# Performance work log

Hardware: AMD Instinct MI355X
Metric: run time of the kernel (lower is better)

Reference implementation:

```python
import jax, jax.numpy as jnp
import numpy as np

NUM_HOSTS = 13


def gcn_conv_max(x, src, dst, n, W, b):
    """PyG GCNConv with aggr='max': x@W, gcn_norm (self-loops + sym norm), max-scatter, +bias.
    src/dst already include self-loop edges."""
    xw = x @ W  # [N, out]
    deg = jnp.zeros((n,), xw.dtype).at[dst].add(1.0)
    dinv = jax.lax.rsqrt(deg)  # deg >= 1 thanks to self-loops
    norm = dinv[src] * dinv[dst]  # [E+N]
    msg = norm[:, None] * xw[src]  # [E+N, out] -- the big gather
    agg = jax.ops.segment_max(msg, dst, num_segments=n)
    return agg + b


def self_attn(v, g, aW, ab, fW, fb, gW, gb):
    """SimpleSelfAttention: softmax over feature dim, weighted-sum over nodes, residual global update."""
    att = jax.nn.softmax(v @ aW + ab, axis=-1)  # [B, Nh, h]
    feat = v @ fW + fb                            # [B, Nh, h]
    out = jnp.sum(att * feat, axis=1)             # [B, h]
    g_ = jnp.concatenate([out, g], axis=-1) @ gW + gb
    return g + g_


def setup_inputs() -> dict:
    key = jax.random.key(0)
    ks = jax.random.split(key, 24)
    IN, H1, H2 = 64, 256, 64
    B, NPG = 256, 200
    N = B * NPG
    E = 409600

    x = jax.random.normal(ks[0], (N, IN), jnp.float32)
    host_idx = (jnp.arange(B)[:, None] * NPG + jnp.arange(NUM_HOSTS)[None, :]).reshape(-1).astype(jnp.int32)
    x = x.at[host_idx, 0].set(1.0)  # hosts = x[:,0]==1
    ei = jax.random.randint(ks[1], (2, E), 0, N, dtype=jnp.int64)

    def lin(k, i, o):
        k1, k2 = jax.random.split(k)
        s = 1.0 / np.sqrt(i)
        return (jax.random.uniform(k1, (i, o), jnp.float32, -s, s),
                jax.random.uniform(k2, (o,), jnp.float32, -s, s))

    W1, b1 = lin(ks[2], IN, H1)
    W2, b2 = lin(ks[3], H1, H2)
    # g0: in=IN, h=H1, g=H1 ; g1: in=H1, h=H1 ; g2: in=H2, h=H2
    a0W, a0b = lin(ks[4], IN, H1); f0W, f0b = lin(ks[5], IN, H1); g0W, g0b = lin(ks[6], H1 + H1, H1)
    a1W, a1b = lin(ks[7], H1, H1); f1W, f1b = lin(ks[8], H1, H1); g1W, g1b = lin(ks[9], H1 + H1, H1)
    a2W, a2b = lin(ks[10], H2, H2); f2W, f2b = lin(ks[11], H2, H2); g2W, g2b = lin(ks[12], H2 + H1, H1)
    o1W, o1b = lin(ks[13], H1, H2)
    o2W, o2b = lin(ks[14], H2, 1)

    return dict(x=x, ei=ei, host_idx=host_idx,
                W1=W1, b1=b1, W2=W2, b2=b2,
                a0W=a0W, a0b=a0b, f0W=f0W, f0b=f0b, g0W=g0W, g0b=g0b,
                a1W=a1W, a1b=a1b, f1W=f1W, f1b=f1b, g1W=g1W, g1b=g1b,
                a2W=a2W, a2b=a2b, f2W=f2W, f2b=f2b, g2W=g2W, g2b=g2b,
                o1W=o1W, o1b=o1b, o2W=o2W, o2b=o2b)


def reference(x, ei, host_idx,
              W1, b1, W2, b2,
              a0W, a0b, f0W, f0b, g0W, g0b,
              a1W, a1b, f1W, f1b, g1W, g1b,
              a2W, a2b, f2W, f2b, g2W, g2b,
              o1W, o1b, o2W, o2b):
    n = x.shape[0]
    B = host_idx.shape[0] // NUM_HOSTS
    loops = jnp.arange(n, dtype=ei.dtype)
    src = jnp.concatenate([ei[0], loops])
    dst = jnp.concatenate([ei[1], loops])

    hx = x[host_idx].reshape(B, NUM_HOSTS, -1)
    g = self_attn(hx, jnp.zeros((B, g0b.shape[0]), x.dtype), a0W, a0b, f0W, f0b, g0W, g0b)

    x1 = jax.nn.relu(gcn_conv_max(x, src, dst, n, W1, b1))
    g = self_attn(x1[host_idx].reshape(B, NUM_HOSTS, -1), g, a1W, a1b, f1W, f1b, g1W, g1b)

    x2 = jax.nn.relu(gcn_conv_max(x1, src, dst, n, W2, b2))
    g = self_attn(x2[host_idx].reshape(B, NUM_HOSTS, -1), g, a2W, a2b, f2W, f2b, g2W, g2b)

    return jax.nn.relu(g @ o1W + o1b) @ o2W + o2b  # [B, 1]
```

## Files before the change

### kernel.cpp

```cpp
#include <hip/hip_runtime.h>
#include <math.h>
#include <stdio.h>

#define N_NODES 51200
#define N_EDGES 409600
#define B_GRAPH 256
#define NH 13

typedef float v4f __attribute__((ext_vector_type(4)));
typedef unsigned v2u __attribute__((ext_vector_type(2)));
__device__ __forceinline__ void nt_store_u2(uint2* p, uint2 v) {
    v2u w; w.x = v.x; w.y = v.y;
    __builtin_nontemporal_store(w, (v2u*)p);
}

__device__ __forceinline__ unsigned pack_bf2(float a, float b) {
    unsigned ua = __float_as_uint(a);
    ua = (ua + 0x7fffu + ((ua >> 16) & 1u)) >> 16;
    unsigned ub = __float_as_uint(b);
    ub = (ub + 0x7fffu + ((ub >> 16) & 1u)) & 0xffff0000u;
    return ua | ub;
}
__device__ __forceinline__ float bf_lo(unsigned u) { return __uint_as_float(u << 16); }
__device__ __forceinline__ float bf_hi(unsigned u) { return __uint_as_float(u & 0xffff0000u); }

__device__ __forceinline__ bool ei_is_64(const int* __restrict__ ei32) {
    int z = 1;
    #pragma unroll
    for (int k = 1; k < 16; k += 2) z &= (ei32[k] == 0);
    return z != 0;
}

__global__ void count_deg(const int* __restrict__ ei32, const long long* __restrict__ ei64,
                          int* __restrict__ degc) {
    int e = blockIdx.x * 256 + threadIdx.x;
    if (e >= N_EDGES) return;
    int v = ei_is_64(ei32) ? (int)ei64[N_EDGES + e] : ei32[N_EDGES + e];
    atomicAdd(&degc[v], 1);
}

__global__ void scan_block_sums(const int* __restrict__ degc, int* __restrict__ bsums) {
    __shared__ int sdata[256];
    int i = blockIdx.x * 256 + threadIdx.x;
    sdata[threadIdx.x] = degc[i];
    __syncthreads();
    for (int s = 128; s > 0; s >>= 1) {
        if (threadIdx.x < s) sdata[threadIdx.x] += sdata[threadIdx.x + s];
        __syncthreads();
    }
    if (threadIdx.x == 0) bsums[blockIdx.x] = sdata[0];
}

__global__ void scan_finalize(int* __restrict__ degc, int* __restrict__ offs,
                              float* __restrict__ dinv, const int* __restrict__ bsums) {
    __shared__ int bs[256];
    __shared__ int s[256];
    const int t = threadIdx.x;
    bs[t] = (t < 200) ? bsums[t] : 0;
    __syncthreads();
    for (int off = 1; off < 256; off <<= 1) {
        int u = (t >= off) ? bs[t - off] : 0;
        __syncthreads();
        bs[t] += u;
        __syncthreads();
    }
    int i = blockIdx.x * 256 + t;
    int cnt = degc[i];
    s[t] = cnt;
    __syncthreads();
    for (int off = 1; off < 256; off <<= 1) {
        int u = (t >= off) ? s[t - off] : 0;
        __syncthreads();
        s[t] += u;
        __syncthreads();
    }
    int base = (blockIdx.x == 0) ? 0 : bs[blockIdx.x - 1];
    int excl = base + s[t] - cnt;
    offs[i] = excl;
    dinv[i] = rsqrtf((float)(cnt + 1));
    degc[i] = excl;
    if (i == N_NODES - 1) offs[N_NODES] = N_EDGES;
}

template <int K, int WS, bool BF16IN>
__device__ __forceinline__ void gemm_body64(const float* __restrict__ X,
        const float* __restrict__ W, const float* __restrict__ bias,
        float* __restrict__ Y, int row0, const int* __restrict__ rows,
        float* __restrict__ xs, float* __restrict__ ws) {
    constexpr int BK = 32;
    constexpr int XS = BK + 4;
    const int t = threadIdx.x;
    const int ct = t & 15;
    const int rt = t >> 4;
    float acc[4][4] = {{0.f}};
    for (int kc = 0; kc < K; kc += BK) {
        __syncthreads();
        #pragma unroll
        for (int i = 0; i < 2; ++i) {
            int idx = t + i * 256;
            int q = idx & 7, r = idx >> 3;
            int xr = rows[r];
            float4 v;
            if (BF16IN) {
                uint2 pv = ((const uint2*)X)[(size_t)xr * (K / 4) + kc / 4 + q];
                v = make_float4(bf_lo(pv.x), bf_hi(pv.x), bf_lo(pv.y), bf_hi(pv.y));
            } else {
                v = *(const float4*)(X + (size_t)xr * K + kc + q * 4);
            }
            *(float4*)&xs[r * XS + q * 4] = v;
        }
        #pragma unroll
        for (int i = 0; i < 2; ++i) {
            int idx = t + i * 256;
            int q = idx & 15, k = idx >> 4;
            float4 v = *(const float4*)(W + (size_t)(kc + k) * WS + q * 4);
            *(float4*)&ws[k * 64 + q * 4] = v;
        }
        __syncthreads();
        #pragma unroll
        for (int kb = 0; kb < BK; kb += 4) {
            float4 wv[4];
            #pragma unroll
            for (int kk = 0; kk < 4; ++kk)
                wv[kk] = *(const float4*)&ws[(kb + kk) * 64 + ct * 4];
            #pragma unroll
            for (int r = 0; r < 4; ++r) {
                float4 xv = *(const float4*)&xs[(rt * 4 + r) * XS + kb];
                float xk[4] = {xv.x, xv.y, xv.z, xv.w};
                #pragma unroll
                for (int kk = 0; kk < 4; ++kk) {
                    acc[r][0] = fmaf(xk[kk], wv[kk].x, acc[r][0]);
                    acc[r][1] = fmaf(xk[kk], wv[kk].y, acc[r][1]);
                    acc[r][2] = fmaf(xk[kk], wv[kk].z, acc[r][2]);
                    acc[r][3] = fmaf(xk[kk], wv[kk].w, acc[r][3]);
                }
            }
        }
    }
    #pragma unroll
    for (int r = 0; r < 4; ++r) {
        int row = row0 + rt * 4 + r;
        float4 o = make_float4(acc[r][0] + bias[ct * 4 + 0],
                               acc[r][1] + bias[ct * 4 + 1],
                               acc[r][2] + bias[ct * 4 + 2],
                               acc[r][3] + bias[ct * 4 + 3]);
        *(float4*)&Y[(size_t)row * 512 + ct * 4] = o;
    }
}

template <int K, int WS, int YS, bool BF16OUT>
__device__ __forceinline__ void gemm_main64(const float* __restrict__ X,
        const float* __restrict__ W, const float* __restrict__ dinv,
        float* __restrict__ Y, int row0,
        float* __restrict__ xs, float* __restrict__ ws) {
    constexpr int BK = 32;
    constexpr int XS = BK + 4;
    const int t = threadIdx.x;
    const int ct = t & 15;
    const int rt = t >> 4;
    float acc[4][4] = {{0.f}};
    for (int kc = 0; kc < K; kc += BK) {
        __syncthreads();
        #pragma unroll
        for (int i = 0; i < 2; ++i) {
            int idx = t + i * 256;
            int q = idx & 7, r = idx >> 3;
            float4 v = *(const float4*)(X + (size_t)(row0 + r) * K + kc + q * 4);
            *(float4*)&xs[r * XS + q * 4] = v;
        }
        #pragma unroll
        for (int i = 0; i < 2; ++i) {
            int idx = t + i * 256;
            int q = idx & 15, k = idx >> 4;
            float4 v = *(const float4*)(W + (size_t)(kc + k) * WS + q * 4);
            *(float4*)&ws[k * 64 + q * 4] = v;
        }
        __syncthreads();
        #pragma unroll
        for (int kb = 0; kb < BK; kb += 4) {
            float4 wv[4];
            #pragma unroll
            for (int kk = 0; kk < 4; ++kk)
                wv[kk] = *(const float4*)&ws[(kb + kk) * 64 + ct * 4];
            #pragma unroll
            for (int r = 0; r < 4; ++r) {
                float4 xv = *(const float4*)&xs[(rt * 4 + r) * XS + kb];
                float xk[4] = {xv.x, xv.y, xv.z, xv.w};
                #pragma unroll
                for (int kk = 0; kk < 4; ++kk) {
                    acc[r][0] = fmaf(xk[kk], wv[kk].x, acc[r][0]);
                    acc[r][1] = fmaf(xk[kk], wv[kk].y, acc[r][1]);
                    acc[r][2] = fmaf(xk[kk], wv[kk].z, acc[r][2]);
                    acc[r][3] = fmaf(xk[kk], wv[kk].w, acc[r][3]);
                }
            }
        }
    }
    #pragma unroll
    for (int r = 0; r < 4; ++r) {
        int row = row0 + rt * 4 + r;
        float sc = dinv[row];
        float4 o = make_float4(acc[r][0] * sc, acc[r][1] * sc,
                               acc[r][2] * sc, acc[r][3] * sc);
        if (BF16OUT) {
            unsigned short* yb = (unsigned short*)Y + (size_t)row * YS;
            uint2 pk;
            pk.x = pack_bf2(o.x, o.y);
            pk.y = pack_bf2(o.z, o.w);
            ((uint2*)yb)[ct] = pk;
        } else {
            *(float4*)&Y[(size_t)row * YS + ct * 4] = o;
        }
    }
}

template <int K, int WS, int YS, int NCOLB, int CPT, bool BF16IN, bool BF16OUT>
__device__ __forceinline__ void gemm_main(const float* __restrict__ X,
        const float* __restrict__ W, const float* __restrict__ dinv,
        float* __restrict__ Y, int row0,
        float* __restrict__ xs, float* __restrict__ ws) {
    constexpr int BK = 32;
    constexpr int XS = BK + 4;
    constexpr int CQ = CPT / 4;
    const int t = threadIdx.x;
    const int ct = t & 15;
    const int rt = t >> 4;
    float acc[8][CPT];
    #pragma unroll
    for (int r = 0; r < 8; ++r)
        #pragma unroll
        for (int c = 0; c < CPT; ++c) acc[r][c] = 0.f;
    for (int kc = 0; kc < K; kc += BK) {
        __syncthreads();
        #pragma unroll
        for (int i = 0; i < 4; ++i) {
            int idx = t + i * 256;
            int q = idx & 7, r = idx >> 3;
            float4 v;
            if (BF16IN) {
                uint2 pv = ((const uint2*)X)[(size_t)(row0 + r) * (K / 4) + kc / 4 + q];
                v = make_float4(bf_lo(pv.x), bf_hi(pv.x), bf_lo(pv.y), bf_hi(pv.y));
            } else {
                v = *(const float4*)(X + (size_t)(row0 + r) * K + kc + q * 4);
            }
            *(float4*)&xs[r * XS + q * 4] = v;
        }
        #pragma unroll
        for (int i = 0; i < NCOLB / 32; ++i) {
            int idx = t + i * 256;
            int q = idx & (NCOLB / 4 - 1), k = idx / (NCOLB / 4);
            float4 v = *(const float4*)(W + (size_t)(kc + k) * WS + q * 4);
            *(float4*)&ws[k * NCOLB + q * 4] = v;
        }
        __syncthreads();
        #pragma unroll
        for (int kb = 0; kb < BK; kb += 4) {
            float4 wv[4][CQ];
            #pragma unroll
            for (int kk = 0; kk < 4; ++kk)
                #pragma unroll
                for (int cq = 0; cq < CQ; ++cq)
                    wv[kk][cq] = *(const float4*)&ws[(kb + kk) * NCOLB + cq * 64 + ct * 4];
            #pragma unroll
            for (int r = 0; r < 8; ++r) {
                float4 xv = *(const float4*)&xs[(rt + 16 * r) * XS + kb];
                float xk[4] = {xv.x, xv.y, xv.z, xv.w};
                #pragma unroll
                for (int kk = 0; kk < 4; ++kk)
                    #pragma unroll
                    for (int cq = 0; cq < CQ; ++cq) {
                        acc[r][cq * 4 + 0] = fmaf(xk[kk], wv[kk][cq].x, acc[r][cq * 4 + 0]);
                        acc[r][cq * 4 + 1] = fmaf(xk[kk], wv[kk][cq].y, acc[r][cq * 4 + 1]);
                        acc[r][cq * 4 + 2] = fmaf(xk[kk], wv[kk][cq].z, acc[r][cq * 4 + 2]);
                        acc[r][cq * 4 + 3] = fmaf(xk[kk], wv[kk][cq].w, acc[r][cq * 4 + 3]);
                    }
            }
        }
    }
    #pragma unroll
    for (int r = 0; r < 8; ++r) {
        int row = row0 + rt + 16 * r;
        float sc = dinv[row];
        #pragma unroll
        for (int cq = 0; cq < CQ; ++cq) {
            float4 o = make_float4(acc[r][cq * 4 + 0] * sc, acc[r][cq * 4 + 1] * sc,
                                   acc[r][cq * 4 + 2] * sc, acc[r][cq * 4 + 3] * sc);
            if (BF16OUT) {
                unsigned short* yb = (unsigned short*)Y + (size_t)row * YS;
                uint2 pk;
                pk.x = pack_bf2(o.x, o.y);
                pk.y = pack_bf2(o.z, o.w);
                ((uint2*)yb)[cq * 16 + ct] = pk;
            } else {
                *(float4*)&Y[(size_t)row * YS + cq * 64 + ct * 4] = o;
            }
        }
    }
}

__global__ __launch_bounds__(256) void fused_gemm1(const float* __restrict__ x,
        const float* __restrict__ W1, float* __restrict__ xw1b,
        const float* __restrict__ dinv,
        const int* __restrict__ ei32, const long long* __restrict__ ei64,
        int* __restrict__ cursor, int* __restrict__ csr,
        const int* __restrict__ host_idx,
        const float* __restrict__ a0W, const float* __restrict__ a0b,
        const float* __restrict__ f0W, const float* __restrict__ f0b,
        float* __restrict__ AF) {
    __shared__ float xs[64 * 36];
    __shared__ float ws[32 * 64];
    __shared__ int rows[64];
    const int bid = blockIdx.x;
    const int t = threadIdx.x;
    if (bid < 3200) {
        const int rb = bid >> 2;
        const int cb = bid & 3;
        gemm_main64<64, 256, 256, true>(
            x, W1 + cb * 64, dinv, xw1b + cb * 32, rb * 64, xs, ws);
    } else if (bid < 3616) {
        const int abid = bid - 3200;
        const int rb = abid >> 3;
        const int cb = abid & 7;
        const int c0 = cb * 64;
        const float* Wp = (c0 < 256) ? (a0W + c0) : (f0W + (c0 - 256));
        const float* bp = (c0 < 256) ? (a0b + c0) : (f0b + (c0 - 256));
        if (t < 64) rows[t] = host_idx[rb * 64 + t];
        __syncthreads();
        gemm_body64<64, 256, false>(x, Wp, bp, AF + c0, rb * 64, rows, xs, ws);
    } else {
        int e = (bid - 3616) * 256 + t;
        if (e < N_EDGES) {
            int u, v;
            if (ei_is_64(ei32)) { u = (int)ei64[e]; v = (int)ei64[N_EDGES + e]; }
            else                { u = ei32[e];      v = ei32[N_EDGES + e]; }
            int pos = atomicAdd(&cursor[v], 1);
            csr[pos] = u;
        }
    }
}

__global__ __launch_bounds__(256) void fused_gemm2(const float* __restrict__ x1b,
        const float* __restrict__ W2, float* __restrict__ xw2,
        const float* __restrict__ dinv,
        const int* __restrict__ host_idx,
        const float* __restrict__ a1W, const float* __restrict__ a1b,
        const float* __restrict__ f1W, const float* __restrict__ f1b,
        float* __restrict__ AF) {
    __shared__ float xs[128 * 36];
    __shared__ float ws[32 * 64];
    __shared__ int rows[64];
    const int bid = blockIdx.x;
    const int t = threadIdx.x;
    if (bid < 400) {
        gemm_main<256, 64, 64, 64, 4, true, false>(
            x1b, W2, dinv, xw2, bid * 128, xs, ws);
    } else {
        const int abid = bid - 400;
        const int rb = abid >> 3;
        const int cb = abid & 7;
        const int c0 = cb * 64;
        const float* Wp = (c0 < 256) ? (a1W + c0) : (f1W + (c0 - 256));
        const float* bp = (c0 < 256) ? (a1b + c0) : (f1b + (c0 - 256));
        if (t < 64) rows[t] = host_idx[rb * 64 + t];
        __syncthreads();
        gemm_body64<256, 256, true>(x1b, Wp, bp, AF + c0, rb * 64, rows, xs, ws);
    }
}

__device__ __forceinline__ void attn_red256(const float* __restrict__ AF,
        const float* __restrict__ gW, const float* __restrict__ gb,
        const float* __restrict__ g_in, float* __restrict__ g_out, int b,
        float (*At)[256], float* red_m, float* red_s, float* cat) {
    const int t = threadIdx.x;
    const int wave = t >> 6, lane = t & 63;
    float accA[NH], accF[NH];
    #pragma unroll
    for (int j = 0; j < NH; ++j) {
        const float* r = AF + (size_t)(b * NH + j) * 512;
        accA[j] = r[t];
        accF[j] = r[256 + t];
        At[j][t] = accA[j];
    }
    __syncthreads();
    for (int j = wave; j < NH; j += 4) {
        float m = -3.402823466e38f;
        #pragma unroll
        for (int q = 0; q < 4; ++q) m = fmaxf(m, At[j][q * 64 + lane]);
        #pragma unroll
        for (int off = 32; off; off >>= 1) m = fmaxf(m, __shfl_xor(m, off));
        if (lane == 0) red_m[j] = m;
    }
    __syncthreads();
    #pragma unroll
    for (int j = 0; j < NH; ++j) At[j][t] = expf(accA[j] - red_m[j]);
    __syncthreads();
    for (int j = wave; j < NH; j += 4) {
        float s = 0.f;
        #pragma unroll
        for (int q = 0; q < 4; ++q) s += At[j][q * 64 + lane];
        #pragma unroll
        for (int off = 32; off; off >>= 1) s += __shfl_xor(s, off);
        if (lane == 0) red_s[j] = s;
    }
    __syncthreads();
    float outc = 0.f;
    #pragma unroll
    for (int j = 0; j < NH; ++j) outc += At[j][t] / red_s[j] * accF[j];
    cat[t] = outc;
    float gv = g_in ? g_in[b * 256 + t] : 0.f;
    cat[256 + t] = gv;
    __syncthreads();
    float acc = gb[t];
    const float* gwp = gW + t;
    #pragma unroll 4
    for (int i4 = 0; i4 < 128; ++i4) {
        float4 cq = ((const float4*)cat)[i4];
        const float* gw4 = gwp + (size_t)i4 * 4 * 256;
        acc = fmaf(cq.x, gw4[0], acc);
        acc = fmaf(cq.y, gw4[256], acc);
        acc = fmaf(cq.z, gw4[512], acc);
        acc = fmaf(cq.w, gw4[768], acc);
    }
    g_out[b * 256 + t] = gv + acc;
}

__global__ __launch_bounds__(256) void fused_agg256(const uint2* __restrict__ xwb,
        const float* __restrict__ dinv, const int* __restrict__ offs,
        const int* __restrict__ csr, const float* __restrict__ bias,
        uint2* __restrict__ outb,
        const float* __restrict__ AF, const float* __restrict__ gW,
        const float* __restrict__ gb, const float* __restrict__ g_in,
        float* __restrict__ g_out) {
    __shared__ float At[NH][256];
    __shared__ float red_m[NH];
    __shared__ float red_s[NH];
    __shared__ float cat[512];
    const int bid = blockIdx.x;
    if (bid < 256) {
        attn_red256(AF, gW, gb, g_in, g_out, bid, At, red_m, red_s, cat);
        return;
    }
    int gid = (bid - 256) * 256 + threadIdx.x;
    int v = gid >> 6;
    int lane = gid & 63;
    uint2 sw = xwb[(size_t)v * 64 + lane];
    float4 acc = make_float4(bf_lo(sw.x), bf_hi(sw.x), bf_lo(sw.y), bf_hi(sw.y));
    int e0 = offs[v];
    int e1 = offs[v + 1];
    int em = e0 + ((e1 - e0) & ~7);
    for (int e = e0; e < em; e += 8) {
        int u[8];
        #pragma unroll
        for (int i = 0; i < 8; ++i) u[i] = csr[e + i];
        uint2 m[8];
        #pragma unroll
        for (int i = 0; i < 8; ++i) m[i] = xwb[(size_t)u[i] * 64 + lane];
        #pragma unroll
        for (int i = 0; i < 8; ++i) {
            acc.x = fmaxf(acc.x, bf_lo(m[i].x));
            acc.y = fmaxf(acc.y, bf_hi(m[i].x));
            acc.z = fmaxf(acc.z, bf_lo(m[i].y));
            acc.w = fmaxf(acc.w, bf_hi(m[i].y));
        }
    }
    if (em < e1) {
        int u[8];
        #pragma unroll
        for (int i = 0; i < 8; ++i) u[i] = csr[(em + i < e1) ? (em + i) : (e1 - 1)];
        uint2 m[8];
        #pragma unroll
        for (int i = 0; i < 8; ++i) m[i] = xwb[(size_t)u[i] * 64 + lane];
        #pragma unroll
        for (int i = 0; i < 8; ++i) {
            if (em + i < e1) {
                acc.x = fmaxf(acc.x, bf_lo(m[i].x));
                acc.y = fmaxf(acc.y, bf_hi(m[i].x));
                acc.z = fmaxf(acc.z, bf_lo(m[i].y));
                acc.w = fmaxf(acc.w, bf_hi(m[i].y));
            }
        }
    }
    float dv = dinv[v];
    float4 b4 = ((const float4*)bias)[lane];
    float4 o;
    o.x = fmaxf(fmaf(acc.x, dv, b4.x), 0.f);
    o.y = fmaxf(fmaf(acc.y, dv, b4.y), 0.f);
    o.z = fmaxf(fmaf(acc.z, dv, b4.z), 0.f);
    o.w = fmaxf(fmaf(acc.w, dv, b4.w), 0.f);
    uint2 pk;
    pk.x = pack_bf2(o.x, o.y);
    pk.y = pack_bf2(o.z, o.w);
    nt_store_u2(outb + (size_t)v * 64 + lane, pk);
}

__global__ __launch_bounds__(1024) void attn_graph_head(
        const float* __restrict__ AF,
        const float* __restrict__ g1W, const float* __restrict__ g1b,
        const float* __restrict__ g_in,
        const float* __restrict__ xw2,
        const float* __restrict__ dinv, const int* __restrict__ offs,
        const int* __restrict__ csr, const float* __restrict__ b2,
        const int* __restrict__ host_idx,
        const float* __restrict__ a2W, const float* __restrict__ a2b,
        const float* __restrict__ f2W, const float* __restrict__ f2b,
        const float* __restrict__ g2W, const float* __restrict__ g2b,
        const float* __restrict__ o1W, const float* __restrict__ o1b,
        const float* __restrict__ o2W, const float* __restrict__ o2b,
        float* __restrict__ out) {
    __shared__ float At[NH][256];
    __shared__ float Ft[NH][256];
    __shared__ float red_m[NH];
    __shared__ float red_s[NH];
    __shared__ float cat[512];
    __shared__ float catB[320];
    __shared__ float g1s[256];
    __shared__ float x2l[NH][64];
    __shared__ float part4[4][256];
    __shared__ float part16[16][64];
    __shared__ float grow[256];
    const int b = blockIdx.x;
    const int t = threadIdx.x;
    const int wave = t >> 6;
    const int lane = t & 63;
    const int c = t & 255;
    const int quad = t >> 8;

    if (wave < NH) {
        int hv = host_idx[b * NH + wave];
        float acc = xw2[(size_t)hv * 64 + lane];
        int e0 = offs[hv], e1 = offs[hv + 1];
        for (int e = e0; e < e1; e += 8) {
            int u[8];
            #pragma unroll
            for (int i = 0; i < 8; ++i) u[i] = csr[(e + i < e1) ? (e + i) : (e1 - 1)];
            float m[8];
            #pragma unroll
            for (int i = 0; i < 8; ++i) m[i] = xw2[(size_t)u[i] * 64 + lane];
            #pragma unroll
            for (int i = 0; i < 8; ++i)
                if (e + i < e1) acc = fmaxf(acc, m[i]);
        }
        x2l[wave][lane] = fmaxf(fmaf(acc, dinv[hv], b2[lane]), 0.f);
    }
    for (int idx = t; idx < NH * 128; idx += 1024) {
        int j = idx >> 7, q = idx & 127;
        float4 v = ((const float4*)(AF + (size_t)(b * NH + j) * 512))[q];
        if (q < 64) *(float4*)&At[j][q * 4] = v;
        else        *(float4*)&Ft[j][(q - 64) * 4] = v;
    }
    __syncthreads();
    if (wave < NH) {
        float m = -3.402823466e38f;
        #pragma unroll
        for (int q = 0; q < 4; ++q) m = fmaxf(m, At[wave][q * 64 + lane]);
        #pragma unroll
        for (int off = 32; off; off >>= 1) m = fmaxf(m, __shfl_xor(m, off));
        if (lane == 0) red_m[wave] = m;
    }
    __syncthreads();
    for (int idx = t; idx < NH * 256; idx += 1024) {
        int j = idx >> 8, cc = idx & 255;
        At[j][cc] = expf(At[j][cc] - red_m[j]);
    }
    __syncthreads();
    if (wave < NH) {
        float s = 0.f;
        #pragma unroll
        for (int q = 0; q < 4; ++q) s += At[wave][q * 64 + lane];
        #pragma unroll
        for (int off = 32; off; off >>= 1) s += __shfl_xor(s, off);
        if (lane == 0) red_s[wave] = s;
    }
    __syncthreads();
    if (quad == 0) {
        float outc = 0.f;
        #pragma unroll
        for (int j = 0; j < NH; ++j) outc += At[j][c] / red_s[j] * Ft[j][c];
        cat[c] = outc;
        cat[256 + c] = g_in[b * 256 + c];
    }
    __syncthreads();
    {
        float acc = 0.f;
        const float* gwp = g1W + c;
        #pragma unroll 4
        for (int i4 = quad * 32; i4 < quad * 32 + 32; ++i4) {
            float4 cq = ((const float4*)cat)[i4];
            const float* gw4 = gwp + (size_t)i4 * 1024;
            acc = fmaf(cq.x, gw4[0], acc);
            acc = fmaf(cq.y, gw4[256], acc);
            acc = fmaf(cq.z, gw4[512], acc);
            acc = fmaf(cq.w, gw4[768], acc);
        }
        part4[quad][c] = acc;
    }
    __syncthreads();
    if (quad == 0)
        g1s[c] = cat[256 + c] + g1b[c] +
                 part4[0][c] + part4[1][c] + part4[2][c] + part4[3][c];
    __syncthreads();
    if (wave < NH) {
        float aA = a2b[lane], aF = f2b[lane];
        #pragma unroll 8
        for (int k = 0; k < 64; ++k) {
            float xv = x2l[wave][k];
            aA = fmaf(xv, a2W[k * 64 + lane], aA);
            aF = fmaf(xv, f2W[k * 64 + lane], aF);
        }
        float m = aA;
        #pragma unroll
        for (int off = 32; off; off >>= 1) m = fmaxf(m, __shfl_xor(m, off));
        float pexp = expf(aA - m);
        float s = pexp;
        #pragma unroll
        for (int off = 32; off; off >>= 1) s += __shfl_xor(s, off);
        At[wave][lane] = pexp / s * aF;
    }
    __syncthreads();
    if (t < 64) {
        float o = 0.f;
        #pragma unroll
        for (int j = 0; j < NH; ++j) o += At[j][t];
        catB[t] = o;
    }
    if (quad == 0) catB[64 + c] = g1s[c];
    __syncthreads();
    {
        float acc = 0.f;
        const float* gwp = g2W + c;
        #pragma unroll 4
        for (int i4 = quad * 20; i4 < quad * 20 + 20; ++i4) {
            float4 cq = ((const float4*)catB)[i4];
            const float* gw4 = gwp + (size_t)i4 * 1024;
            acc = fmaf(cq.x, gw4[0], acc);
            acc = fmaf(cq.y, gw4[256], acc);
            acc = fmaf(cq.z, gw4[512], acc);
            acc = fmaf(cq.w, gw4[768], acc);
        }
        part4[quad][c] = acc;
    }
    __syncthreads();
    if (quad == 0)
        grow[c] = g1s[c] + g2b[c] +
                  part4[0][c] + part4[1][c] + part4[2][c] + part4[3][c];
    __syncthreads();
    {
        float hp = 0.f;
        #pragma unroll
        for (int k = wave * 16; k < wave * 16 + 16; ++k)
            hp = fmaf(grow[k], o1W[(size_t)k * 64 + lane], hp);
        part16[wave][lane] = hp;
    }
    __syncthreads();
    if (wave == 0) {
        float h = o1b[lane];
        #pragma unroll
        for (int w = 0; w < 16; ++w) h += part16[w][lane];
        h = fmaxf(h, 0.f);
        float sres = h * o2W[lane];
        #pragma unroll
        for (int off = 32; off; off >>= 1) sres += __shfl_xor(sres, off);
        if (lane == 0) out[b] = sres + o2b[0];
    }
}

extern "C" void kernel_launch(void* const* d_in, const int* in_sizes, int n_in,
                              void* d_out, int out_size, void* d_ws, size_t ws_size,
                              hipStream_t stream) {
    (void)in_sizes; (void)n_in; (void)out_size;
    const float* x    = (const float*)d_in[0];
    const int* ei32   = (const int*)d_in[1];
    const long long* ei64 = (const long long*)d_in[1];
    const int* hidx   = (const int*)d_in[2];
    const float* W1 = (const float*)d_in[3],  *b1 = (const float*)d_in[4];
    const float* W2 = (const float*)d_in[5],  *b2 = (const float*)d_in[6];
    const float* a0W = (const float*)d_in[7],  *a0b = (const float*)d_in[8];
    const float* f0W = (const float*)d_in[9],  *f0b = (const float*)d_in[10];
    const float* g0W = (const float*)d_in[11], *g0b = (const float*)d_in[12];
    const float* a1W = (const float*)d_in[13], *a1b = (const float*)d_in[14];
    const float* f1W = (const float*)d_in[15], *f1b = (const float*)d_in[16];
    const float* g1W = (const float*)d_in[17], *g1b = (const float*)d_in[18];
    const float* a2W = (const float*)d_in[19], *a2b = (const float*)d_in[20];
    const float* f2W = (const float*)d_in[21], *f2b = (const float*)d_in[22];
    const float* g2W = (const float*)d_in[23], *g2b = (const float*)d_in[24];
    const float* o1W = (const float*)d_in[25], *o1b = (const float*)d_in[26];
    const float* o2W = (const float*)d_in[27], *o2b = (const float*)d_in[28];
    float* outp = (float*)d_out;

    char* p = (char*)d_ws;
    auto alloc = [&](size_t bytes) {
        char* r = p;
        p += (bytes + 255) & ~(size_t)255;
        return r;
    };
    float* dinv = (float*)alloc((size_t)N_NODES * 4);
    int* degc   = (int*)alloc((size_t)N_NODES * 4);
    int* offs   = (int*)alloc((size_t)(N_NODES + 1) * 4);
    int* csr    = (int*)alloc((size_t)N_EDGES * 4);
    int* bsums  = (int*)alloc(256 * 4);
    float* g    = (float*)alloc((size_t)B_GRAPH * 256 * 4);
    float* AF   = (float*)alloc((size_t)B_GRAPH * NH * 512 * 4);
    unsigned short* xw1b = (unsigned short*)alloc((size_t)N_NODES * 256 * 2);
    unsigned short* x1b  = (unsigned short*)alloc((size_t)N_NODES * 256 * 2);
    float* xw2  = (float*)alloc((size_t)N_NODES * 64 * 4);

    size_t need = (size_t)(p - (char*)d_ws);
    if (need > ws_size) {
        fprintf(stderr, "kernel_launch: ws too small (%zu needed, %zu have)\n", need, ws_size);
        return;
    }

    (void)hipMemsetAsync(degc, 0, (size_t)N_NODES * 4, stream);
    count_deg<<<1600, 256, 0, stream>>>(ei32, ei64, degc);
    scan_block_sums<<<200, 256, 0, stream>>>(degc, bsums);
    scan_finalize<<<200, 256, 0, stream>>>(degc, offs, dinv, bsums);

    fused_gemm1<<<5216, 256, 0, stream>>>(
        x, W1, (float*)xw1b, dinv, ei32, ei64, degc, csr,
        hidx, a0W, a0b, f0W, f0b, AF);
    fused_agg256<<<256 + 12800, 256, 0, stream>>>((const uint2*)xw1b, dinv, offs, csr,
                                                  b1, (uint2*)x1b, AF, g0W, g0b,
                                                  nullptr, g);
    fused_gemm2<<<816, 256, 0, stream>>>(
        (const float*)x1b, W2, xw2, dinv, hidx, a1W, a1b, f1W, f1b, AF);
    attn_graph_head<<<256, 1024, 0, stream>>>(
        AF, g1W, g1b, g, xw2, dinv, offs, csr, b2, hidx,
        a2W, a2b, f2W, f2b, g2W, g2b, o1W, o1b, o2W, o2b, outp);
}
```

Measured before the change: 289.2 us.

## Use bf16 MFMA with hi/lo split for the two node GEMMs

Replaces the scalar FP32 FMA tiling in the X@W1 and X1@W2 node GEMMs with 16x16x32 bf16 MFMA instructions. Near-FP32 accuracy is kept by splitting operands into bf16 high and low parts (three products for GEMM1; two for GEMM2, whose input is already bf16). The weights are pre-split and pre-swizzled into fragment order by extra blocks appended to the degree-count kernel. Results are staged through shared memory so global stores are coalesced. This removes FP32 ALU work in exchange for a small extra prep pass and slightly different rounding.

```diff
diff --git a/kernel.cpp b/kernel.cpp
--- a/kernel.cpp
+++ b/kernel.cpp
@@ -9,6 +9,9 @@
 
 typedef float v4f __attribute__((ext_vector_type(4)));
 typedef unsigned v2u __attribute__((ext_vector_type(2)));
+typedef short s16x8 __attribute__((ext_vector_type(8)));
+typedef float f32x4 __attribute__((ext_vector_type(4)));
+
 __device__ __forceinline__ void nt_store_u2(uint2* p, uint2 v) {
     v2u w; w.x = v.x; w.y = v.y;
     __builtin_nontemporal_store(w, (v2u*)p);
@@ -24,6 +27,27 @@
 __device__ __forceinline__ float bf_lo(unsigned u) { return __uint_as_float(u << 16); }
 __device__ __forceinline__ float bf_hi(unsigned u) { return __uint_as_float(u & 0xffff0000u); }
 
+__device__ __forceinline__ s16x8 as_s8(uint4 u) {
+    return __builtin_bit_cast(s16x8, u);
+}
+__device__ __forceinline__ f32x4 mfma16(s16x8 a, s16x8 b, f32x4 c) {
+    return __builtin_amdgcn_mfma_f32_16x16x32_bf16(a, b, c, 0, 0, 0);
+}
+
+__device__ __forceinline__ void cvt_hilo(const float4& xa, const float4& xb,
+                                         s16x8& hi, s16x8& lo) {
+    unsigned h0 = pack_bf2(xa.x, xa.y);
+    unsigned h1 = pack_bf2(xa.z, xa.w);
+    unsigned h2 = pack_bf2(xb.x, xb.y);
+    unsigned h3 = pack_bf2(xb.z, xb.w);
+    unsigned l0 = pack_bf2(xa.x - bf_lo(h0), xa.y - bf_hi(h0));
+    unsigned l1 = pack_bf2(xa.z - bf_lo(h1), xa.w - bf_hi(h1));
+    unsigned l2 = pack_bf2(xb.x - bf_lo(h2), xb.y - bf_hi(h2));
+    unsigned l3 = pack_bf2(xb.z - bf_lo(h3), xb.w - bf_hi(h3));
+    hi = as_s8(make_uint4(h0, h1, h2, h3));
+    lo = as_s8(make_uint4(l0, l1, l2, l3));
+}
+
 __device__ __forceinline__ bool ei_is_64(const int* __restrict__ ei32) {
     int z = 1;
     #pragma unroll
@@ -32,8 +56,45 @@
 }
 
 __global__ void count_deg(const int* __restrict__ ei32, const long long* __restrict__ ei64,
-                          int* __restrict__ degc) {
-    int e = blockIdx.x * 256 + threadIdx.x;
+                          int* __restrict__ degc,
+                          const float* __restrict__ W1, const float* __restrict__ W2,
+                          uint4* __restrict__ w1h, uint4* __restrict__ w1l,
+                          uint4* __restrict__ w2h, uint4* __restrict__ w2l) {
+    const int bid = blockIdx.x;
+    if (bid >= 1600) {
+        int rec = (bid - 1600) * 256 + threadIdx.x;
+        bool isW1 = rec < 2048;
+        int r = isW1 ? rec : rec - 2048;
+        int l = r & 63;
+        int lg = l >> 4;
+        int col, krow, N;
+        const float* W;
+        if (isW1) {
+            int c = r >> 7; int s = (r >> 6) & 1;
+            col = c * 16 + (l & 15); krow = s * 32 + lg * 4; W = W1; N = 256;
+        } else {
+            int c = r >> 9; int s = (r >> 6) & 7;
+            col = c * 16 + (l & 15); krow = s * 32 + lg * 4; W = W2; N = 64;
+        }
+        float f[8];
+        #pragma unroll
+        for (int e = 0; e < 8; ++e) {
+            int kk = krow + (e & 3) + 16 * (e >> 2);
+            f[e] = W[(size_t)kk * N + col];
+        }
+        unsigned h[4], lo[4];
+        #pragma unroll
+        for (int p = 0; p < 4; ++p) {
+            h[p] = pack_bf2(f[2 * p], f[2 * p + 1]);
+            lo[p] = pack_bf2(f[2 * p] - bf_lo(h[p]), f[2 * p + 1] - bf_hi(h[p]));
+        }
+        uint4 H = make_uint4(h[0], h[1], h[2], h[3]);
+        uint4 L = make_uint4(lo[0], lo[1], lo[2], lo[3]);
+        if (isW1) { w1h[r] = H; w1l[r] = L; }
+        else      { w2h[r] = H; w2l[r] = L; }
+        return;
+    }
+    int e = bid * 256 + threadIdx.x;
     if (e >= N_EDGES) return;
     int v = ei_is_64(ei32) ? (int)ei64[N_EDGES + e] : ei32[N_EDGES + e];
     atomicAdd(&degc[v], 1);
@@ -148,177 +209,77 @@
     }
 }
 
-template <int K, int WS, int YS, bool BF16OUT>
-__device__ __forceinline__ void gemm_main64(const float* __restrict__ X,
-        const float* __restrict__ W, const float* __restrict__ dinv,
-        float* __restrict__ Y, int row0,
-        float* __restrict__ xs, float* __restrict__ ws) {
-    constexpr int BK = 32;
-    constexpr int XS = BK + 4;
-    const int t = threadIdx.x;
-    const int ct = t & 15;
-    const int rt = t >> 4;
-    float acc[4][4] = {{0.f}};
-    for (int kc = 0; kc < K; kc += BK) {
-        __syncthreads();
-        #pragma unroll
-        for (int i = 0; i < 2; ++i) {
-            int idx = t + i * 256;
-            int q = idx & 7, r = idx >> 3;
-            float4 v = *(const float4*)(X + (size_t)(row0 + r) * K + kc + q * 4);
-            *(float4*)&xs[r * XS + q * 4] = v;
-        }
-        #pragma unroll
-        for (int i = 0; i < 2; ++i) {
-            int idx = t + i * 256;
-            int q = idx & 15, k = idx >> 4;
-            float4 v = *(const float4*)(W + (size_t)(kc + k) * WS + q * 4);
-            *(float4*)&ws[k * 64 + q * 4] = v;
-        }
-        __syncthreads();
-        #pragma unroll
-        for (int kb = 0; kb < BK; kb += 4) {
-            float4 wv[4];
-            #pragma unroll
-            for (int kk = 0; kk < 4; ++kk)
-                wv[kk] = *(const float4*)&ws[(kb + kk) * 64 + ct * 4];
-            #pragma unroll
-            for (int r = 0; r < 4; ++r) {
-                float4 xv = *(const float4*)&xs[(rt * 4 + r) * XS + kb];
-                float xk[4] = {xv.x, xv.y, xv.z, xv.w};
-                #pragma unroll
-                for (int kk = 0; kk < 4; ++kk) {
-                    acc[r][0] = fmaf(xk[kk], wv[kk].x, acc[r][0]);
-                    acc[r][1] = fmaf(xk[kk], wv[kk].y, acc[r][1]);
-                    acc[r][2] = fmaf(xk[kk], wv[kk].z, acc[r][2]);
-                    acc[r][3] = fmaf(xk[kk], wv[kk].w, acc[r][3]);
-                }
-            }
-        }
-    }
-    #pragma unroll
-    for (int r = 0; r < 4; ++r) {
-        int row = row0 + rt * 4 + r;
-        float sc = dinv[row];
-        float4 o = make_float4(acc[r][0] * sc, acc[r][1] * sc,
-                               acc[r][2] * sc, acc[r][3] * sc);
-        if (BF16OUT) {
-            unsigned short* yb = (unsigned short*)Y + (size_t)row * YS;
-            uint2 pk;
-            pk.x = pack_bf2(o.x, o.y);
-            pk.y = pack_bf2(o.z, o.w);
-            ((uint2*)yb)[ct] = pk;
-        } else {
-            *(float4*)&Y[(size_t)row * YS + ct * 4] = o;
-        }
-    }
-}
-
-template <int K, int WS, int YS, int NCOLB, int CPT, bool BF16IN, bool BF16OUT>
-__device__ __forceinline__ void gemm_main(const float* __restrict__ X,
-        const float* __restrict__ W, const float* __restrict__ dinv,
-        float* __restrict__ Y, int row0,
-        float* __restrict__ xs, float* __restrict__ ws) {
-    constexpr int BK = 32;
-    constexpr int XS = BK + 4;
-    constexpr int CQ = CPT / 4;
-    const int t = threadIdx.x;
-    const int ct = t & 15;
-    const int rt = t >> 4;
-    float acc[8][CPT];
-    #pragma unroll
-    for (int r = 0; r < 8; ++r)
-        #pragma unroll
-        for (int c = 0; c < CPT; ++c) acc[r][c] = 0.f;
-    for (int kc = 0; kc < K; kc += BK) {
-        __syncthreads();
-        #pragma unroll
-        for (int i = 0; i < 4; ++i) {
-            int idx = t + i * 256;
-            int q = idx & 7, r = idx >> 3;
-            float4 v;
-            if (BF16IN) {
-                uint2 pv = ((const uint2*)X)[(size_t)(row0 + r) * (K / 4) + kc / 4 + q];
-                v = make_float4(bf_lo(pv.x), bf_hi(pv.x), bf_lo(pv.y), bf_hi(pv.y));
-            } else {
-                v = *(const float4*)(X + (size_t)(row0 + r) * K + kc + q * 4);
-            }
-            *(float4*)&xs[r * XS + q * 4] = v;
-        }
-        #pragma unroll
-        for (int i = 0; i < NCOLB / 32; ++i) {
-            int idx = t + i * 256;
-            int q = idx & (NCOLB / 4 - 1), k = idx / (NCOLB / 4);
-            float4 v = *(const float4*)(W + (size_t)(kc + k) * WS + q * 4);
-            *(float4*)&ws[k * NCOLB + q * 4] = v;
-        }
-        __syncthreads();
-        #pragma unroll
-        for (int kb = 0; kb < BK; kb += 4) {
-            float4 wv[4][CQ];
-            #pragma unroll
-            for (int kk = 0; kk < 4; ++kk)
-                #pragma unroll
-                for (int cq = 0; cq < CQ; ++cq)
-                    wv[kk][cq] = *(const float4*)&ws[(kb + kk) * NCOLB + cq * 64 + ct * 4];
-            #pragma unroll
-            for (int r = 0; r < 8; ++r) {
-                float4 xv = *(const float4*)&xs[(rt + 16 * r) * XS + kb];
-                float xk[4] = {xv.x, xv.y, xv.z, xv.w};
-                #pragma unroll
-                for (int kk = 0; kk < 4; ++kk)
-                    #pragma unroll
-                    for (int cq = 0; cq < CQ; ++cq) {
-                        acc[r][cq * 4 + 0] = fmaf(xk[kk], wv[kk][cq].x, acc[r][cq * 4 + 0]);
-                        acc[r][cq * 4 + 1] = fmaf(xk[kk], wv[kk][cq].y, acc[r][cq * 4 + 1]);
-                        acc[r][cq * 4 + 2] = fmaf(xk[kk], wv[kk][cq].z, acc[r][cq * 4 + 2]);
-                        acc[r][cq * 4 + 3] = fmaf(xk[kk], wv[kk][cq].w, acc[r][cq * 4 + 3]);
-                    }
-            }
-        }
-    }
-    #pragma unroll
-    for (int r = 0; r < 8; ++r) {
-        int row = row0 + rt + 16 * r;
-        float sc = dinv[row];
-        #pragma unroll
-        for (int cq = 0; cq < CQ; ++cq) {
-            float4 o = make_float4(acc[r][cq * 4 + 0] * sc, acc[r][cq * 4 + 1] * sc,
-                                   acc[r][cq * 4 + 2] * sc, acc[r][cq * 4 + 3] * sc);
-            if (BF16OUT) {
-                unsigned short* yb = (unsigned short*)Y + (size_t)row * YS;
-                uint2 pk;
-                pk.x = pack_bf2(o.x, o.y);
-                pk.y = pack_bf2(o.z, o.w);
-                ((uint2*)yb)[cq * 16 + ct] = pk;
-            } else {
-                *(float4*)&Y[(size_t)row * YS + cq * 64 + ct * 4] = o;
-            }
-        }
-    }
-}
-
-__global__ __launch_bounds__(256) void fused_gemm1(const float* __restrict__ x,
-        const float* __restrict__ W1, float* __restrict__ xw1b,
-        const float* __restrict__ dinv,
+__global__ __launch_bounds__(256, 4) void fused_gemm1(const float* __restrict__ x,
+        const uint4* __restrict__ w1h, const uint4* __restrict__ w1l,
+        float* __restrict__ xw1b, const float* __restrict__ dinv,
         const int* __restrict__ ei32, const long long* __restrict__ ei64,
         int* __restrict__ cursor, int* __restrict__ csr,
         const int* __restrict__ host_idx,
         const float* __restrict__ a0W, const float* __restrict__ a0b,
         const float* __restrict__ f0W, const float* __restrict__ f0b,
         float* __restrict__ AF) {
-    __shared__ float xs[64 * 36];
-    __shared__ float ws[32 * 64];
+    __shared__ float smem[64 * 68];
     __shared__ int rows[64];
     const int bid = blockIdx.x;
     const int t = threadIdx.x;
-    if (bid < 3200) {
-        const int rb = bid >> 2;
-        const int cb = bid & 3;
-        gemm_main64<64, 256, 256, true>(
-            x, W1 + cb * 64, dinv, xw1b + cb * 32, rb * 64, xs, ws);
-    } else if (bid < 3616) {
-        const int abid = bid - 3200;
+    if (bid < 1600) {
+        const int row0 = (bid >> 2) * 128;
+        const int c0 = (bid & 3) * 64;
+        const int w = t >> 6, l = t & 63, lr = l & 15, lg = l >> 4;
+        f32x4 acc[2][4] = {};
+        #pragma unroll
+        for (int s = 0; s < 2; ++s) {
+            s16x8 bh[4], bl[4];
+            #pragma unroll
+            for (int cc = 0; cc < 4; ++cc) {
+                int idx = (((c0 >> 4) + cc) * 2 + s) * 64 + l;
+                bh[cc] = as_s8(w1h[idx]);
+                bl[cc] = as_s8(w1l[idx]);
+            }
+            #pragma unroll
+            for (int f = 0; f < 2; ++f) {
+                int rowA = row0 + w * 32 + f * 16 + lr;
+                const float* xp = x + (size_t)rowA * 64 + s * 32 + lg * 4;
+                float4 xa = *(const float4*)xp;
+                float4 xb = *(const float4*)(xp + 16);
+                s16x8 ah, al;
+                cvt_hilo(xa, xb, ah, al);
+                #pragma unroll
+                for (int cc = 0; cc < 4; ++cc) {
+                    acc[f][cc] = mfma16(ah, bh[cc], acc[f][cc]);
+                    acc[f][cc] = mfma16(al, bh[cc], acc[f][cc]);
+                    acc[f][cc] = mfma16(ah, bl[cc], acc[f][cc]);
+                }
+            }
+        }
+        #pragma unroll
+        for (int f = 0; f < 2; ++f) {
+            if (f) __syncthreads();
+            #pragma unroll
+            for (int r = 0; r < 4; ++r) {
+                float dv = dinv[row0 + w * 32 + f * 16 + lg * 4 + r];
+                #pragma unroll
+                for (int cc = 0; cc < 4; ++cc)
+                    smem[(w * 16 + lg * 4 + r) * 68 + cc * 16 + lr] = acc[f][cc][r] * dv;
+            }
+            __syncthreads();
+            int row_l = t >> 2, cB = (t & 3) * 16;
+            int grow = row0 + (row_l >> 4) * 32 + f * 16 + (row_l & 15);
+            const float* src = &smem[row_l * 68 + cB];
+            float4 v0 = *(const float4*)(src + 0);
+            float4 v1 = *(const float4*)(src + 4);
+            float4 v2 = *(const float4*)(src + 8);
+            float4 v3 = *(const float4*)(src + 12);
+            uint4 o0, o1;
+            o0.x = pack_bf2(v0.x, v0.y); o0.y = pack_bf2(v0.z, v0.w);
+            o0.z = pack_bf2(v1.x, v1.y); o0.w = pack_bf2(v1.z, v1.w);
+            o1.x = pack_bf2(v2.x, v2.y); o1.y = pack_bf2(v2.z, v2.w);
+            o1.z = pack_bf2(v3.x, v3.y); o1.w = pack_bf2(v3.z, v3.w);
+            uint4* yp = (uint4*)xw1b + (size_t)grow * 32 + (c0 >> 3) + (t & 3) * 2;
+            yp[0] = o0; yp[1] = o1;
+        }
+    } else if (bid < 2016) {
+        const int abid = bid - 1600;
         const int rb = abid >> 3;
         const int cb = abid & 7;
         const int c0 = cb * 64;
@@ -326,9 +287,9 @@
         const float* bp = (c0 < 256) ? (a0b + c0) : (f0b + (c0 - 256));
         if (t < 64) rows[t] = host_idx[rb * 64 + t];
         __syncthreads();
-        gemm_body64<64, 256, false>(x, Wp, bp, AF + c0, rb * 64, rows, xs, ws);
+        gemm_body64<64, 256, false>(x, Wp, bp, AF + c0, rb * 64, rows, smem, smem + 64 * 36);
     } else {
-        int e = (bid - 3616) * 256 + t;
+        int e = (bid - 2016) * 256 + t;
         if (e < N_EDGES) {
             int u, v;
             if (ei_is_64(ei32)) { u = (int)ei64[e]; v = (int)ei64[N_EDGES + e]; }
@@ -339,21 +300,65 @@
     }
 }
 
-__global__ __launch_bounds__(256) void fused_gemm2(const float* __restrict__ x1b,
-        const float* __restrict__ W2, float* __restrict__ xw2,
-        const float* __restrict__ dinv,
+__global__ __launch_bounds__(256, 4) void fused_gemm2(const float* __restrict__ x1b,
+        const uint4* __restrict__ w2h, const uint4* __restrict__ w2l,
+        float* __restrict__ xw2, const float* __restrict__ dinv,
         const int* __restrict__ host_idx,
         const float* __restrict__ a1W, const float* __restrict__ a1b,
         const float* __restrict__ f1W, const float* __restrict__ f1b,
         float* __restrict__ AF) {
-    __shared__ float xs[128 * 36];
-    __shared__ float ws[32 * 64];
+    __shared__ float smem[64 * 68];
     __shared__ int rows[64];
     const int bid = blockIdx.x;
     const int t = threadIdx.x;
     if (bid < 400) {
-        gemm_main<256, 64, 64, 64, 4, true, false>(
-            x1b, W2, dinv, xw2, bid * 128, xs, ws);
+        const int row0 = bid * 128;
+        const int w = t >> 6, l = t & 63, lr = l & 15, lg = l >> 4;
+        f32x4 acc[2][4] = {};
+        const uint2* xb = (const uint2*)x1b;
+        #pragma unroll 2
+        for (int s = 0; s < 8; ++s) {
+            s16x8 bh[4], bl[4];
+            #pragma unroll
+            for (int cc = 0; cc < 4; ++cc) {
+                int idx = (cc * 8 + s) * 64 + l;
+                bh[cc] = as_s8(w2h[idx]);
+                bl[cc] = as_s8(w2l[idx]);
+            }
+            #pragma unroll
+            for (int f = 0; f < 2; ++f) {
+                int row = row0 + w * 32 + f * 16 + lr;
+                const uint2* ap = xb + (size_t)row * 64 + s * 8 + lg;
+                uint2 a0 = ap[0];
+                uint2 a1 = ap[4];
+                s16x8 a = as_s8(make_uint4(a0.x, a0.y, a1.x, a1.y));
+                #pragma unroll
+                for (int cc = 0; cc < 4; ++cc) {
+                    acc[f][cc] = mfma16(a, bh[cc], acc[f][cc]);
+                    acc[f][cc] = mfma16(a, bl[cc], acc[f][cc]);
+                }
+            }
+        }
+        #pragma unroll
+        for (int f = 0; f < 2; ++f) {
+            if (f) __syncthreads();
+            #pragma unroll
+            for (int r = 0; r < 4; ++r) {
+                float dv = dinv[row0 + w * 32 + f * 16 + lg * 4 + r];
+                #pragma unroll
+                for (int cc = 0; cc < 4; ++cc)
+                    smem[(w * 16 + lg * 4 + r) * 68 + cc * 16 + lr] = acc[f][cc][r] * dv;
+            }
+            __syncthreads();
+            int row_l = t >> 2, cB = (t & 3) * 16;
+            int grow = row0 + (row_l >> 4) * 32 + f * 16 + (row_l & 15);
+            const float* src = &smem[row_l * 68 + cB];
+            float4* dstp = (float4*)(xw2 + (size_t)grow * 64 + cB);
+            dstp[0] = *(const float4*)(src + 0);
+            dstp[1] = *(const float4*)(src + 4);
+            dstp[2] = *(const float4*)(src + 8);
+            dstp[3] = *(const float4*)(src + 12);
+        }
     } else {
         const int abid = bid - 400;
         const int rb = abid >> 3;
@@ -363,7 +368,7 @@
         const float* bp = (c0 < 256) ? (a1b + c0) : (f1b + (c0 - 256));
         if (t < 64) rows[t] = host_idx[rb * 64 + t];
         __syncthreads();
-        gemm_body64<256, 256, true>(x1b, Wp, bp, AF + c0, rb * 64, rows, xs, ws);
+        gemm_body64<256, 256, true>(x1b, Wp, bp, AF + c0, rb * 64, rows, smem, smem + 64 * 36);
     }
 }
 
@@ -703,6 +708,10 @@
     unsigned short* xw1b = (unsigned short*)alloc((size_t)N_NODES * 256 * 2);
     unsigned short* x1b  = (unsigned short*)alloc((size_t)N_NODES * 256 * 2);
     float* xw2  = (float*)alloc((size_t)N_NODES * 64 * 4);
+    uint4* w1h  = (uint4*)alloc((size_t)2048 * 16);
+    uint4* w1l  = (uint4*)alloc((size_t)2048 * 16);
+    uint4* w2h  = (uint4*)alloc((size_t)2048 * 16);
+    uint4* w2l  = (uint4*)alloc((size_t)2048 * 16);
 
     size_t need = (size_t)(p - (char*)d_ws);
     if (need > ws_size) {
@@ -711,18 +720,18 @@
     }
 
     (void)hipMemsetAsync(degc, 0, (size_t)N_NODES * 4, stream);
-    count_deg<<<1600, 256, 0, stream>>>(ei32, ei64, degc);
+    count_deg<<<1616, 256, 0, stream>>>(ei32, ei64, degc, W1, W2, w1h, w1l, w2h, w2l);
     scan_block_sums<<<200, 256, 0, stream>>>(degc, bsums);
     scan_finalize<<<200, 256, 0, stream>>>(degc, offs, dinv, bsums);
 
-    fused_gemm1<<<5216, 256, 0, stream>>>(
-        x, W1, (float*)xw1b, dinv, ei32, ei64, degc, csr,
+    fused_gemm1<<<3616, 256, 0, stream>>>(
+        x, w1h, w1l, (float*)xw1b, dinv, ei32, ei64, degc, csr,
         hidx, a0W, a0b, f0W, f0b, AF);
     fused_agg256<<<256 + 12800, 256, 0, stream>>>((const uint2*)xw1b, dinv, offs, csr,
                                                   b1, (uint2*)x1b, AF, g0W, g0b,
                                                   nullptr, g);
     fused_gemm2<<<816, 256, 0, stream>>>(
-        (const float*)x1b, W2, xw2, dinv, hidx, a1W, a1b, f1W, f1b, AF);
+        (const float*)x1b, w2h, w2l, xw2, dinv, hidx, a1W, a1b, f1W, f1b, AF);
     attn_graph_head<<<256, 1024, 0, stream>>>(
         AF, g1W, g1b, g, xw2, dinv, offs, csr, b2, hidx,
         a2W, a2b, f2W, f2b, g2W, g2b, o1W, o1b, o2W, o2b, outp);
```

New measurement: 271.4 us. 6.1% less time.
